# Kernel optimization log

Hardware: AMD Instinct MI355X
Metric: run time of the kernel (lower is better)

## Reference

```python
import jax, jax.numpy as jnp
import numpy as np

EPS = 1e-5


def _selective_scan(u, delta, A, Bm, Cm, D, delta_bias):
    # u, delta: (B, KD, L); A: (KD, N); Bm, Cm: (B, K, N, L); D, delta_bias: (KD,)
    Bb, KD, L = u.shape
    K = Bm.shape[1]
    Din = KD // K
    N = A.shape[1]
    delta = jax.nn.softplus(delta + delta_bias[None, :, None])            # (B,KD,L)
    dA = jnp.exp(delta[..., None] * A[None, :, None, :])                  # (B,KD,L,N)
    Bl = jnp.broadcast_to(Bm[:, :, None], (Bb, K, Din, N, L)).reshape(Bb, KD, N, L)
    Bl = jnp.moveaxis(Bl, -1, 2)                                          # (B,KD,L,N)
    dBu = (delta * u)[..., None] * Bl                                     # (B,KD,L,N)

    def comb(c1, c2):
        a1, b1 = c1
        a2, b2 = c2
        return a2 * a1, a2 * b1 + b2

    _, h = jax.lax.associative_scan(comb, (dA, dBu), axis=2)              # h: (B,KD,L,N)
    Cl = jnp.broadcast_to(Cm[:, :, None], (Bb, K, Din, N, L)).reshape(Bb, KD, N, L)
    Cl = jnp.moveaxis(Cl, -1, 2)
    y = jnp.sum(h * Cl, axis=-1) + D[None, :, None] * u                   # (B,KD,L)
    return y


def setup_inputs() -> dict:
    key = jax.random.key(0)
    ks = jax.random.split(key, 12)
    B, H, W, Dd = 1, 16, 16, 16
    C = 48            # d_model
    Din = 48          # d_inner (expand=1)
    N = 16            # d_state
    R = 3             # dt_rank = ceil(48/16)
    K = 8             # scan directions
    x = jax.random.normal(ks[0], (B, H, W, Dd, C), jnp.float32)
    in_proj_w = jax.random.normal(ks[1], (2 * Din, C), jnp.float32) * (C ** -0.5)
    conv_w = jax.random.normal(ks[2], (Din, 1, 3, 3, 3), jnp.float32) * 0.1
    conv_b = jax.random.normal(ks[3], (Din,), jnp.float32) * 0.01
    x_proj_weight = jax.random.normal(ks[4], (K, R + 2 * N, Din), jnp.float32) * (Din ** -0.5)
    dt_projs_weight = jax.random.uniform(ks[5], (K, Din, R), jnp.float32, -(R ** -0.5), R ** -0.5)
    # faithful dt bias init: inverse softplus of dt ~ logU(1e-3, 1e-1)
    u = jax.random.uniform(ks[6], (K, Din), jnp.float32)
    dt = jnp.exp(u * (np.log(0.1) - np.log(0.001)) + np.log(0.001))
    dt = jnp.clip(dt, 1e-4, None)
    dt_projs_bias = dt + jnp.log(-jnp.expm1(-dt))
    A_logs = jnp.log(jnp.broadcast_to(jnp.arange(1, N + 1, dtype=jnp.float32), (K * Din, N))).copy()
    Ds = jnp.ones((K * Din,), jnp.float32)
    norm_w = jnp.ones((Din,), jnp.float32)
    norm_b = jnp.zeros((Din,), jnp.float32)
    out_proj_w = jax.random.normal(ks[7], (C, Din), jnp.float32) * (Din ** -0.5)
    return {"x": x, "in_proj_w": in_proj_w, "conv_w": conv_w, "conv_b": conv_b,
            "x_proj_weight": x_proj_weight, "dt_projs_weight": dt_projs_weight,
            "dt_projs_bias": dt_projs_bias, "A_logs": A_logs, "Ds": Ds,
            "norm_w": norm_w, "norm_b": norm_b, "out_proj_w": out_proj_w}


def reference(x, in_proj_w, conv_w, conv_b, x_proj_weight, dt_projs_weight,
              dt_projs_bias, A_logs, Ds, norm_w, norm_b, out_proj_w):
    Bb, H, W, Dd, C = x.shape
    Din = in_proj_w.shape[0] // 2
    K = x_proj_weight.shape[0]
    R = dt_projs_weight.shape[2]
    N = A_logs.shape[1]
    L = H * W * Dd
    # in_proj and gate split
    xz = jnp.einsum('bhwdc,ec->bhwde', x, in_proj_w)
    xm, z = jnp.split(xz, 2, axis=-1)
    # depthwise 3D conv + SiLU (channels-first)
    xc = jnp.transpose(xm, (0, 4, 1, 2, 3))                               # (B,Din,H,W,D)
    xc = jax.lax.conv_general_dilated(xc, conv_w, (1, 1, 1), 'SAME',
                                      dimension_numbers=('NCDHW', 'OIDHW', 'NCDHW'),
                                      feature_group_count=Din)
    xc = jax.nn.silu(xc + conv_b[None, :, None, None, None])
    # 8 scan orderings: 4 axis permutations + their reversals
    x0 = xc.reshape(Bb, Din, L)
    x1 = jnp.transpose(xc, (0, 1, 3, 2, 4)).reshape(Bb, Din, L)
    x2 = jnp.transpose(xc, (0, 1, 4, 3, 2)).reshape(Bb, Din, L)
    x3 = jnp.transpose(xc, (0, 1, 2, 4, 3)).reshape(Bb, Din, L)
    x4s = jnp.stack([x0, x1, x2, x3], axis=1)                             # (B,4,Din,L)
    xs = jnp.concatenate([x4s, jnp.flip(x4s, axis=-1)], axis=1)           # (B,8,Din,L)
    # per-direction projections
    x_dbl = jnp.einsum('bkdl,kcd->bkcl', xs, x_proj_weight)
    dts, Bs, Cs = jnp.split(x_dbl, [R, R + N], axis=2)                    # (B,K,R,L),(B,K,N,L),(B,K,N,L)
    dts = jnp.einsum('bkrl,kdr->bkdl', dts, dt_projs_weight)              # (B,K,Din,L)
    u = xs.reshape(Bb, K * Din, L)
    delta = dts.reshape(Bb, K * Din, L)
    A = -jnp.exp(A_logs)                                                  # (K*Din, N)
    y = _selective_scan(u, delta, A, Bs, Cs, Ds, dt_projs_bias.reshape(-1))
    y = y.reshape(Bb, K, Din, L)
    # undo reversals and permutations, sum all directions
    yk = y[:, :4] + jnp.flip(y[:, 4:], axis=-1)                           # (B,4,Din,L)
    y0 = yk[:, 0].reshape(Bb, Din, H, W, Dd)
    y1 = jnp.transpose(yk[:, 1].reshape(Bb, Din, W, H, Dd), (0, 1, 3, 2, 4))
    y2 = jnp.transpose(yk[:, 2].reshape(Bb, Din, Dd, W, H), (0, 1, 4, 3, 2))
    y3 = jnp.transpose(yk[:, 3].reshape(Bb, Din, H, Dd, W), (0, 1, 2, 4, 3))
    ysum = y0 + y1 + y2 + y3                                              # (B,Din,H,W,D)
    # LayerNorm over channels, gate, out_proj
    yl = jnp.transpose(ysum, (0, 2, 3, 4, 1))                             # (B,H,W,D,Din)
    mu = jnp.mean(yl, axis=-1, keepdims=True)
    var = jnp.mean((yl - mu) ** 2, axis=-1, keepdims=True)
    yn = (yl - mu) * jax.lax.rsqrt(var + EPS) * norm_w + norm_b
    out = yn * jax.nn.silu(z)
    return jnp.einsum('bhwde,ce->bhwdc', out, out_proj_w)
```

## Files before the change

### kernel.cpp

```cpp
#include <hip/hip_runtime.h>
#include <hip/hip_bf16.h>
#include <math.h>

#define HH 16
#define WW 16
#define DD 16
#define LL 4096
#define CC 48
#define DIN 48
#define NN 16
#define RR 3
#define KK 8
#define KD 384
#define NCH 64
#define CHL 64

__device__ __forceinline__ float dpp_add(float x, const int ctrl_tag) {
    int xi = __float_as_int(x);
    int yi;
    switch (ctrl_tag) {
        case 0: yi = __builtin_amdgcn_update_dpp(0, xi, 0xB1, 0xF, 0xF, true); break;
        case 1: yi = __builtin_amdgcn_update_dpp(0, xi, 0x4E, 0xF, 0xF, true); break;
        case 2: yi = __builtin_amdgcn_update_dpp(0, xi, 0x124, 0xF, 0xF, true); break;
        default: yi = __builtin_amdgcn_update_dpp(0, xi, 0x128, 0xF, 0xF, true); break;
    }
    return x + __int_as_float(yi);
}
__device__ __forceinline__ float row16_sum(float p) {
    p = dpp_add(p, 0);
    p = dpp_add(p, 1);
    p = dpp_add(p, 2);
    p = dpp_add(p, 3);
    return p;
}

__global__ __launch_bounds__(256) void k_inproj(const float* __restrict__ x,
                                                const float* __restrict__ W,
                                                float* __restrict__ xm,
                                                float* __restrict__ z) {
    int tid = blockIdx.x * 256 + threadIdx.x;
    if (tid >= LL * 96) return;
    int e = tid % 96, l = tid / 96;
    const float4* xr = (const float4*)(x + l * CC);
    const float4* wr = (const float4*)(W + e * CC);
    float acc = 0.f;
#pragma unroll
    for (int c4 = 0; c4 < CC / 4; ++c4) {
        float4 a = xr[c4], b = wr[c4];
        acc += a.x * b.x + a.y * b.y + a.z * b.z + a.w * b.w;
    }
    if (e < DIN) xm[e * LL + l] = acc;
    else         z[l * DIN + (e - DIN)] = acc;
}

__global__ __launch_bounds__(256) void k_conv(const float* __restrict__ xm,
                                              const float* __restrict__ cw,
                                              const float* __restrict__ cb,
                                              float* __restrict__ xc) {
    int tid = blockIdx.x * 256 + threadIdx.x;
    if (tid >= DIN * LL) return;
    int s = tid & (LL - 1), d = tid >> 12;
    int dd = s & 15, w = (s >> 4) & 15, h = s >> 8;
    const float* wp = cw + d * 27;
    const float* xp = xm + d * LL;
    float acc = 0.f;
#pragma unroll
    for (int i = -1; i <= 1; ++i) {
        int hh = h + i; if (hh < 0 || hh > 15) continue;
#pragma unroll
        for (int j = -1; j <= 1; ++j) {
            int ww2 = w + j; if (ww2 < 0 || ww2 > 15) continue;
#pragma unroll
            for (int q = -1; q <= 1; ++q) {
                int dd2 = dd + q; if (dd2 < 0 || dd2 > 15) continue;
                acc += wp[(i + 1) * 9 + (j + 1) * 3 + (q + 1)]
                     * xp[hh * 256 + ww2 * 16 + dd2];
            }
        }
    }
    acc += cb[d];
    xc[tid] = acc / (1.f + __expf(-acc));
}

__global__ __launch_bounds__(768) void k_xscan1(const float* __restrict__ xc,
                                                const float* __restrict__ xpw,
                                                const float* __restrict__ dtw,
                                                const float* __restrict__ dtb,
                                                const float* __restrict__ A_logs,
                                                float* __restrict__ BC,
                                                float* __restrict__ ud_g,
                                                float* __restrict__ pa_g,
                                                float* __restrict__ hf_g) {
    int k = blockIdx.x >> 6;
    int c = blockIdx.x & (NCH - 1);
    int l0 = c * CHL;
    int tid = threadIdx.x;
    __shared__ float xt[48 * 68];
    __shared__ float xd[35 * 65];
    __shared__ float2 ud[48 * 68];
    int kperm = k & 3, krev = k & 4;
#pragma unroll
    for (int r = 0; r < 4; ++r) {
        int item = r * 768 + tid;
        int d = item >> 6, i = item & 63;
        int lg = l0 + i;
        int ll = krev ? (LL - 1 - lg) : lg;
        int a = ll >> 8, b2 = (ll >> 4) & 15, c2 = ll & 15;
        int src;
        switch (kperm) {
            case 0: src = ll;                       break;
            case 1: src = b2 * 256 + a * 16 + c2;   break;
            case 2: src = c2 * 256 + b2 * 16 + a;   break;
            default: src = a * 256 + c2 * 16 + b2;  break;
        }
        xt[d * 68 + i] = xc[d * LL + src];
    }
    __syncthreads();
    if (tid < 560) {
        int cc = tid % 35, l4 = tid / 35;
        const float* wr = xpw + (k * 35 + cc) * DIN;
        float4 acc = {0.f, 0.f, 0.f, 0.f};
#pragma unroll
        for (int d2 = 0; d2 < 48; ++d2) {
            float4 v = ((const float4*)(xt + d2 * 68))[l4];
            float w = wr[d2];
            acc.x += v.x * w; acc.y += v.y * w; acc.z += v.z * w; acc.w += v.w * w;
        }
        float* o = xd + cc * 65 + l4 * 4;
        o[0] = acc.x; o[1] = acc.y; o[2] = acc.z; o[3] = acc.w;
    }
    __syncthreads();
    if (tid < 512) {
        int l = tid >> 3, q = tid & 7;
        float4 v;
#pragma unroll
        for (int j = 0; j < 4; ++j) (&v.x)[j] = xd[(3 + q * 4 + j) * 65 + l];
        ((float4*)(BC + ((size_t)(k * LL + l0 + l)) * 32))[q] = v;
    }
#pragma unroll
    for (int r = 0; r < 4; ++r) {
        int item = r * 768 + tid;
        int d2 = item >> 6, l = item & 63;
        int gd = k * DIN + d2;
        float v = xd[l] * dtw[gd * 3] + xd[65 + l] * dtw[gd * 3 + 1]
                + xd[130 + l] * dtw[gd * 3 + 2] + dtb[gd];
        float sp = (v > 20.f) ? v : log1pf(__expf(v));
        float u = xt[d2 * 68 + l];
        float2 p = make_float2(u, sp);
        ud[d2 * 68 + l] = p;
        ((float2*)ud_g)[(size_t)gd * LL + l0 + l] = p;
    }
    __syncthreads();
    int d = tid >> 4, n = tid & 15;
    int gid = k * DIN + d;
    float A = -__expf(A_logs[gid * NN + n]);
    float h = 0.f, pa = 1.f;
#pragma unroll 8
    for (int i = 0; i < CHL; ++i) {
        float2 uv = ud[d * 68 + i];
        float Bv = xd[(3 + n) * 65 + i];
        float dA = __expf(uv.y * A);
        h = h * dA + uv.y * uv.x * Bv;
        pa *= dA;
    }
    size_t si = (size_t)gid * (NCH * 16) + c * 16 + n;
    pa_g[si] = pa;
    hf_g[si] = h;
}

__global__ __launch_bounds__(256) void k_scan2(const float* __restrict__ pa_g,
                                               const float* __restrict__ hf_g,
                                               float* __restrict__ h0_g) {
    int t = blockIdx.x * 256 + threadIdx.x;
    if (t >= KD * NN) return;
    int n = t & 15;
    int gid = t >> 4;
    size_t base = (size_t)gid * (NCH * 16) + n;
    float h = 0.f;
#pragma unroll 4
    for (int c = 0; c < NCH; ++c) {
        size_t idx = base + (size_t)c * 16;
        h0_g[idx] = h;
        h = h * pa_g[idx] + hf_g[idx];
    }
}

__global__ __launch_bounds__(768) void k_scan3(const float* __restrict__ ud_g,
                                               const float* __restrict__ BC,
                                               const float* __restrict__ A_logs,
                                               const float* __restrict__ Ds,
                                               const float* __restrict__ h0_g,
                                               float* __restrict__ y2) {
    int k = blockIdx.x >> 6;
    int c = blockIdx.x & (NCH - 1);
    int l0 = c * CHL;
    int tid = threadIdx.x;
    int d = tid >> 4, n = tid & 15;
    int gid = k * DIN + d;
    __shared__ float y_t[48 * 68];
    float A = -__expf(A_logs[gid * NN + n]);
    float Dv = Ds[gid];
    float h = h0_g[(size_t)gid * (NCH * 16) + c * 16 + n];
    const float2* up = ((const float2*)ud_g) + (size_t)gid * LL + l0;
    const float* bp = BC + ((size_t)(k * LL + l0)) * 32 + n;
    const float* cp = bp + 16;
#pragma unroll 8
    for (int i = 0; i < CHL; ++i) {
        float2 uv = up[i];
        float Bv = bp[(size_t)i * 32];
        float Cv = cp[(size_t)i * 32];
        float dA = __expf(uv.y * A);
        h = h * dA + uv.y * uv.x * Bv;
        float p = row16_sum(h * Cv);
        if (n == 0) y_t[d * 68 + i] = p + Dv * uv.x;
    }
    __syncthreads();
    {
        int g = tid >> 6, l = tid & 63;
        int lg = l0 + l;
        int ll = (k & 4) ? (LL - 1 - lg) : lg;
        int a = ll >> 8, b2 = (ll >> 4) & 15, c2 = ll & 15;
        int s;
        switch (k & 3) {
            case 0: s = ll;                        break;
            case 1: s = b2 * 256 + a * 16 + c2;    break;
            case 2: s = c2 * 256 + b2 * 16 + a;    break;
            default: s = a * 256 + c2 * 16 + b2;   break;
        }
        float4 v;
#pragma unroll
        for (int j = 0; j < 4; ++j) (&v.x)[j] = y_t[(g * 4 + j) * 68 + l];
        ((float4*)(y2 + (size_t)s * KD + k * DIN))[g] = v;
    }
}

__global__ __launch_bounds__(256) void k_final2(const float* __restrict__ y2,
                                                const float* __restrict__ z,
                                                const float* __restrict__ nw,
                                                const float* __restrict__ nb,
                                                const float* __restrict__ opw,
                                                float* __restrict__ out) {
    int wv = threadIdx.x >> 6, lane = threadIdx.x & 63;
    int s = blockIdx.x * 4 + wv;
    __shared__ float g[4][DIN];
    float val = 0.f;
    if (lane < DIN) {
        const float* yp = y2 + (size_t)s * KD + lane;
#pragma unroll
        for (int k = 0; k < KK; ++k) val += yp[k * DIN];
    }
    float m = val;
#pragma unroll
    for (int o = 32; o >= 1; o >>= 1) m += __shfl_xor(m, o, 64);
    m *= (1.f / 48.f);
    float dv = (lane < DIN) ? (val - m) : 0.f;
    float v2 = dv * dv;
#pragma unroll
    for (int o = 32; o >= 1; o >>= 1) v2 += __shfl_xor(v2, o, 64);
    v2 *= (1.f / 48.f);
    float inv = rsqrtf(v2 + 1e-5f);
    if (lane < DIN) {
        float yn = dv * inv * nw[lane] + nb[lane];
        float zz = z[s * DIN + lane];
        g[wv][lane] = yn * (zz / (1.f + __expf(-zz)));
    }
    __syncthreads();
    if (lane < DIN) {
        const float* wr = opw + lane * DIN;
        float acc = 0.f;
#pragma unroll
        for (int e = 0; e < DIN; ++e) acc += g[wv][e] * wr[e];
        out[s * CC + lane] = acc;
    }
}

extern "C" void kernel_launch(void* const* d_in, const int* in_sizes, int n_in,
                              void* d_out, int out_size, void* d_ws, size_t ws_size,
                              hipStream_t stream) {
    const float* x      = (const float*)d_in[0];
    const float* ipw    = (const float*)d_in[1];
    const float* cw     = (const float*)d_in[2];
    const float* cb     = (const float*)d_in[3];
    const float* xpw    = (const float*)d_in[4];
    const float* dtw    = (const float*)d_in[5];
    const float* dtb    = (const float*)d_in[6];
    const float* A_logs = (const float*)d_in[7];
    const float* Ds     = (const float*)d_in[8];
    const float* nw     = (const float*)d_in[9];
    const float* nb     = (const float*)d_in[10];
    const float* opw    = (const float*)d_in[11];
    float* out = (float*)d_out;

    float* ws   = (float*)d_ws;
    float* xm   = ws;
    float* z    = xm + DIN * LL;
    float* xc   = z + LL * DIN;
    float* ud_g = xc + DIN * LL;
    float* BC   = ud_g + (size_t)2 * KD * LL;
    float* y2   = BC + (size_t)KK * LL * 32;
    float* pa_g = y2 + (size_t)LL * KD;
    float* hf_g = pa_g + (size_t)KD * NCH * 16;
    float* h0_g = hf_g + (size_t)KD * NCH * 16;

    k_inproj<<<(LL * 96 + 255) / 256, 256, 0, stream>>>(x, ipw, xm, z);
    k_conv<<<(DIN * LL + 255) / 256, 256, 0, stream>>>(xm, cw, cb, xc);
    k_xscan1<<<KK * NCH, 768, 0, stream>>>(xc, xpw, dtw, dtb, A_logs,
                                           BC, ud_g, pa_g, hf_g);
    k_scan2<<<(KD * NN + 255) / 256, 256, 0, stream>>>(pa_g, hf_g, h0_g);
    k_scan3<<<KK * NCH, 768, 0, stream>>>(ud_g, BC, A_logs, Ds, h0_g, y2);
    k_final2<<<LL / 4, 256, 0, stream>>>(y2, z, nw, nb, opw, out);
}
```

Before: 155.0 us.

## Fuse all stages into one cooperative persistent kernel with grid syncs

Replaces six separate kernel launches with a single cooperative kernel of 512 blocks × 256 threads that runs in-projection, conv, x-projection plus chunk scan, the inter-chunk scan, the output scan and the final norm/gate/projection, separated by grid.sync. The scan's B/C and u/delta now stay in shared memory between the chunk-prefix pass and the output pass instead of going through global buffers, and each thread handles three channels rather than one. It is meant to remove launch overhead and global round-trips. In exchange it costs grid-wide barriers and less parallelism per stage, with a fallback to the old multi-kernel path if the cooperative launch fails.

```diff
diff --git a/kernel.cpp b/kernel.cpp
--- a/kernel.cpp
+++ b/kernel.cpp
@@ -1,6 +1,9 @@
 #include <hip/hip_runtime.h>
 #include <hip/hip_bf16.h>
+#include <hip/hip_cooperative_groups.h>
 #include <math.h>
+
+namespace cg = cooperative_groups;
 
 #define HH 16
 #define WW 16
@@ -14,6 +17,8 @@
 #define KD 384
 #define NCH 64
 #define CHL 64
+#define NBLK (KK * NCH)
+#define NTHR 256
 
 __device__ __forceinline__ float dpp_add(float x, const int ctrl_tag) {
     int xi = __float_as_int(x);
@@ -32,6 +37,279 @@
     p = dpp_add(p, 2);
     p = dpp_add(p, 3);
     return p;
+}
+
+__device__ __forceinline__ int perm_src(int kperm, int ll) {
+    int a = ll >> 8, b2 = (ll >> 4) & 15, c2 = ll & 15;
+    switch (kperm) {
+        case 0: return ll;
+        case 1: return b2 * 256 + a * 16 + c2;
+        case 2: return c2 * 256 + b2 * 16 + a;
+        default: return a * 256 + c2 * 16 + b2;
+    }
+}
+
+__global__ __launch_bounds__(NTHR) void k_all(const float* __restrict__ x,
+                                              const float* __restrict__ ipw,
+                                              const float* __restrict__ cw,
+                                              const float* __restrict__ cb,
+                                              const float* __restrict__ xpw,
+                                              const float* __restrict__ dtw,
+                                              const float* __restrict__ dtb,
+                                              const float* __restrict__ A_logs,
+                                              const float* __restrict__ Ds,
+                                              const float* __restrict__ nw,
+                                              const float* __restrict__ nb,
+                                              const float* __restrict__ opw,
+                                              float* __restrict__ out,
+                                              float* __restrict__ xm,
+                                              float* __restrict__ z,
+                                              float* __restrict__ xc,
+                                              float* __restrict__ y2,
+                                              float* __restrict__ pa_g,
+                                              float* __restrict__ hf_g,
+                                              float* __restrict__ h0_g) {
+    cg::grid_group grid = cg::this_grid();
+    int tid = threadIdx.x;
+    int bid = blockIdx.x;
+    __shared__ float xt[48 * 68];
+    __shared__ float xd[35 * 65];
+    __shared__ float2 ud[48 * 68];
+    __shared__ float gbuf[4][49];
+
+    {
+        int base = bid * 768;
+#pragma unroll
+        for (int r = 0; r < 3; ++r) {
+            int item = base + r * NTHR + tid;
+            int e = item % 96, l = item / 96;
+            const float4* xr = (const float4*)(x + l * CC);
+            const float4* wr = (const float4*)(ipw + e * CC);
+            float acc = 0.f;
+#pragma unroll
+            for (int c4 = 0; c4 < CC / 4; ++c4) {
+                float4 a = xr[c4], b = wr[c4];
+                acc += a.x * b.x + a.y * b.y + a.z * b.z + a.w * b.w;
+            }
+            if (e < DIN) xm[e * LL + l] = acc;
+            else         z[l * DIN + (e - DIN)] = acc;
+        }
+    }
+    grid.sync();
+
+    {
+        int base = bid * 384;
+#pragma unroll
+        for (int r = 0; r < 2; ++r) {
+            int li = r * NTHR + tid;
+            if (li < 384) {
+                int item = base + li;
+                int s = item & (LL - 1), d = item >> 12;
+                int dd = s & 15, w = (s >> 4) & 15, h = s >> 8;
+                const float* wp = cw + d * 27;
+                const float* xp = xm + d * LL;
+                float acc = 0.f;
+#pragma unroll
+                for (int i = -1; i <= 1; ++i) {
+                    int hh = h + i; if (hh < 0 || hh > 15) continue;
+#pragma unroll
+                    for (int j = -1; j <= 1; ++j) {
+                        int ww2 = w + j; if (ww2 < 0 || ww2 > 15) continue;
+#pragma unroll
+                        for (int q = -1; q <= 1; ++q) {
+                            int dd2 = dd + q; if (dd2 < 0 || dd2 > 15) continue;
+                            acc += wp[(i + 1) * 9 + (j + 1) * 3 + (q + 1)]
+                                 * xp[hh * 256 + ww2 * 16 + dd2];
+                        }
+                    }
+                }
+                acc += cb[d];
+                xc[item] = acc / (1.f + __expf(-acc));
+            }
+        }
+    }
+    grid.sync();
+
+    int k = bid >> 6;
+    int c = bid & (NCH - 1);
+    int l0 = c * CHL;
+    int kperm = k & 3, krev = k & 4;
+    {
+#pragma unroll
+        for (int r = 0; r < 12; ++r) {
+            int item = r * NTHR + tid;
+            int d = item >> 6, i = item & 63;
+            int lg = l0 + i;
+            int ll = krev ? (LL - 1 - lg) : lg;
+            xt[d * 68 + i] = xc[d * LL + perm_src(kperm, ll)];
+        }
+        __syncthreads();
+#pragma unroll
+        for (int r = 0; r < 3; ++r) {
+            int item = r * NTHR + tid;
+            if (item < 560) {
+                int cc = item % 35, l4 = item / 35;
+                const float* wr = xpw + (k * 35 + cc) * DIN;
+                float4 acc = {0.f, 0.f, 0.f, 0.f};
+#pragma unroll
+                for (int d2 = 0; d2 < 48; ++d2) {
+                    float4 v = ((const float4*)(xt + d2 * 68))[l4];
+                    float w = wr[d2];
+                    acc.x += v.x * w; acc.y += v.y * w; acc.z += v.z * w; acc.w += v.w * w;
+                }
+                float* o = xd + cc * 65 + l4 * 4;
+                o[0] = acc.x; o[1] = acc.y; o[2] = acc.z; o[3] = acc.w;
+            }
+        }
+        __syncthreads();
+#pragma unroll
+        for (int r = 0; r < 12; ++r) {
+            int item = r * NTHR + tid;
+            int d2 = item >> 6, l = item & 63;
+            int gd = k * DIN + d2;
+            float v = xd[l] * dtw[gd * 3] + xd[65 + l] * dtw[gd * 3 + 1]
+                    + xd[130 + l] * dtw[gd * 3 + 2] + dtb[gd];
+            float sp = (v > 20.f) ? v : log1pf(__expf(v));
+            ud[d2 * 68 + l] = make_float2(xt[d2 * 68 + l], sp);
+        }
+        __syncthreads();
+        int n = tid & 15, dbase = tid >> 4;
+        float A0 = -__expf(A_logs[(k * DIN + dbase) * NN + n]);
+        float A1 = -__expf(A_logs[(k * DIN + dbase + 16) * NN + n]);
+        float A2 = -__expf(A_logs[(k * DIN + dbase + 32) * NN + n]);
+        float h0v = 0.f, h1v = 0.f, h2v = 0.f;
+        float p0v = 1.f, p1v = 1.f, p2v = 1.f;
+#pragma unroll 4
+        for (int i = 0; i < CHL; ++i) {
+            float Bv = xd[(3 + n) * 65 + i];
+            float2 u0 = ud[dbase * 68 + i];
+            float2 u1 = ud[(dbase + 16) * 68 + i];
+            float2 u2 = ud[(dbase + 32) * 68 + i];
+            float dA0 = __expf(u0.y * A0);
+            float dA1 = __expf(u1.y * A1);
+            float dA2 = __expf(u2.y * A2);
+            h0v = h0v * dA0 + u0.y * u0.x * Bv;
+            h1v = h1v * dA1 + u1.y * u1.x * Bv;
+            h2v = h2v * dA2 + u2.y * u2.x * Bv;
+            p0v *= dA0; p1v *= dA1; p2v *= dA2;
+        }
+        pa_g[((size_t)(k * DIN + dbase) * 16 + n) * NCH + c] = p0v;
+        pa_g[((size_t)(k * DIN + dbase + 16) * 16 + n) * NCH + c] = p1v;
+        pa_g[((size_t)(k * DIN + dbase + 32) * 16 + n) * NCH + c] = p2v;
+        hf_g[((size_t)(k * DIN + dbase) * 16 + n) * NCH + c] = h0v;
+        hf_g[((size_t)(k * DIN + dbase + 16) * 16 + n) * NCH + c] = h1v;
+        hf_g[((size_t)(k * DIN + dbase + 32) * 16 + n) * NCH + c] = h2v;
+    }
+    grid.sync();
+
+    {
+        int wavebase = bid * 4 + (tid >> 6);
+        int lane = tid & 63;
+#pragma unroll
+        for (int j = 0; j < 3; ++j) {
+            int wid = j * 2048 + wavebase;
+            size_t idx = (size_t)wid * NCH + lane;
+            float a = pa_g[idx], b = hf_g[idx];
+#pragma unroll
+            for (int o = 1; o < 64; o <<= 1) {
+                float ap = __shfl_up(a, o, 64);
+                float bp = __shfl_up(b, o, 64);
+                if (lane >= o) { b = a * bp + b; a = a * ap; }
+            }
+            float h0 = __shfl_up(b, 1, 64);
+            if (lane == 0) h0 = 0.f;
+            h0_g[idx] = h0;
+        }
+    }
+    grid.sync();
+
+    {
+        int n = tid & 15, dbase = tid >> 4;
+        float A0 = -__expf(A_logs[(k * DIN + dbase) * NN + n]);
+        float A1 = -__expf(A_logs[(k * DIN + dbase + 16) * NN + n]);
+        float A2 = -__expf(A_logs[(k * DIN + dbase + 32) * NN + n]);
+        float D0 = Ds[k * DIN + dbase];
+        float D1 = Ds[k * DIN + dbase + 16];
+        float D2 = Ds[k * DIN + dbase + 32];
+        float h0v = h0_g[((size_t)(k * DIN + dbase) * 16 + n) * NCH + c];
+        float h1v = h0_g[((size_t)(k * DIN + dbase + 16) * 16 + n) * NCH + c];
+        float h2v = h0_g[((size_t)(k * DIN + dbase + 32) * 16 + n) * NCH + c];
+        float* y_t = xt;
+#pragma unroll 4
+        for (int i = 0; i < CHL; ++i) {
+            float Bv = xd[(3 + n) * 65 + i];
+            float Cv = xd[(19 + n) * 65 + i];
+            float2 u0 = ud[dbase * 68 + i];
+            float2 u1 = ud[(dbase + 16) * 68 + i];
+            float2 u2 = ud[(dbase + 32) * 68 + i];
+            float dA0 = __expf(u0.y * A0);
+            float dA1 = __expf(u1.y * A1);
+            float dA2 = __expf(u2.y * A2);
+            h0v = h0v * dA0 + u0.y * u0.x * Bv;
+            h1v = h1v * dA1 + u1.y * u1.x * Bv;
+            h2v = h2v * dA2 + u2.y * u2.x * Bv;
+            float s0 = row16_sum(h0v * Cv);
+            float s1 = row16_sum(h1v * Cv);
+            float s2 = row16_sum(h2v * Cv);
+            if (n == 0) {
+                y_t[dbase * 68 + i] = s0 + D0 * u0.x;
+                y_t[(dbase + 16) * 68 + i] = s1 + D1 * u1.x;
+                y_t[(dbase + 32) * 68 + i] = s2 + D2 * u2.x;
+            }
+        }
+        __syncthreads();
+#pragma unroll
+        for (int r = 0; r < 3; ++r) {
+            int item = r * NTHR + tid;
+            int g = item >> 6, l = item & 63;
+            int lg = l0 + l;
+            int ll = krev ? (LL - 1 - lg) : lg;
+            int s = perm_src(kperm, ll);
+            float4 v;
+#pragma unroll
+            for (int j = 0; j < 4; ++j) (&v.x)[j] = y_t[(g * 4 + j) * 68 + l];
+            ((float4*)(y2 + (size_t)s * KD + k * DIN))[g] = v;
+        }
+    }
+    grid.sync();
+
+    {
+        int wv = tid >> 6, lane = tid & 63;
+#pragma unroll
+        for (int r = 0; r < 2; ++r) {
+            int s = bid * 8 + wv * 2 + r;
+            float val = 0.f;
+            if (lane < DIN) {
+                const float* yp = y2 + (size_t)s * KD + lane;
+#pragma unroll
+                for (int kk = 0; kk < KK; ++kk) val += yp[kk * DIN];
+            }
+            float m = val;
+#pragma unroll
+            for (int o = 32; o >= 1; o >>= 1) m += __shfl_xor(m, o, 64);
+            m *= (1.f / 48.f);
+            float dv = (lane < DIN) ? (val - m) : 0.f;
+            float v2 = dv * dv;
+#pragma unroll
+            for (int o = 32; o >= 1; o >>= 1) v2 += __shfl_xor(v2, o, 64);
+            v2 *= (1.f / 48.f);
+            float inv = rsqrtf(v2 + 1e-5f);
+            if (lane < DIN) {
+                float yn = dv * inv * nw[lane] + nb[lane];
+                float zz = z[s * DIN + lane];
+                gbuf[wv][lane] = yn * (zz / (1.f + __expf(-zz)));
+            }
+            __syncthreads();
+            if (lane < DIN) {
+                const float* wr = opw + lane * DIN;
+                float acc = 0.f;
+#pragma unroll
+                for (int e = 0; e < DIN; ++e) acc += gbuf[wv][e] * wr[e];
+                out[s * CC + lane] = acc;
+            }
+            __syncthreads();
+        }
+    }
 }
 
 __global__ __launch_bounds__(256) void k_inproj(const float* __restrict__ x,
@@ -105,15 +383,7 @@
         int d = item >> 6, i = item & 63;
         int lg = l0 + i;
         int ll = krev ? (LL - 1 - lg) : lg;
-        int a = ll >> 8, b2 = (ll >> 4) & 15, c2 = ll & 15;
-        int src;
-        switch (kperm) {
-            case 0: src = ll;                       break;
-            case 1: src = b2 * 256 + a * 16 + c2;   break;
-            case 2: src = c2 * 256 + b2 * 16 + a;   break;
-            default: src = a * 256 + c2 * 16 + b2;  break;
-        }
-        xt[d * 68 + i] = xc[d * LL + src];
+        xt[d * 68 + i] = xc[d * LL + perm_src(kperm, ll)];
     }
     __syncthreads();
     if (tid < 560) {
@@ -215,23 +485,14 @@
         if (n == 0) y_t[d * 68 + i] = p + Dv * uv.x;
     }
     __syncthreads();
-    {
-        int g = tid >> 6, l = tid & 63;
-        int lg = l0 + l;
-        int ll = (k & 4) ? (LL - 1 - lg) : lg;
-        int a = ll >> 8, b2 = (ll >> 4) & 15, c2 = ll & 15;
-        int s;
-        switch (k & 3) {
-            case 0: s = ll;                        break;
-            case 1: s = b2 * 256 + a * 16 + c2;    break;
-            case 2: s = c2 * 256 + b2 * 16 + a;    break;
-            default: s = a * 256 + c2 * 16 + b2;   break;
-        }
-        float4 v;
-#pragma unroll
-        for (int j = 0; j < 4; ++j) (&v.x)[j] = y_t[(g * 4 + j) * 68 + l];
-        ((float4*)(y2 + (size_t)s * KD + k * DIN))[g] = v;
-    }
+    int g = tid >> 6, l = tid & 63;
+    int lg = l0 + l;
+    int ll = (k & 4) ? (LL - 1 - lg) : lg;
+    int s = perm_src(k & 3, ll);
+    float4 v;
+#pragma unroll
+    for (int j = 0; j < 4; ++j) (&v.x)[j] = y_t[(g * 4 + j) * 68 + l];
+    ((float4*)(y2 + (size_t)s * KD + k * DIN))[g] = v;
 }
 
 __global__ __launch_bounds__(256) void k_final2(const float* __restrict__ y2,
@@ -295,18 +556,28 @@
     float* xm   = ws;
     float* z    = xm + DIN * LL;
     float* xc   = z + LL * DIN;
-    float* ud_g = xc + DIN * LL;
-    float* BC   = ud_g + (size_t)2 * KD * LL;
-    float* y2   = BC + (size_t)KK * LL * 32;
+    float* y2   = xc + DIN * LL;
     float* pa_g = y2 + (size_t)LL * KD;
     float* hf_g = pa_g + (size_t)KD * NCH * 16;
     float* h0_g = hf_g + (size_t)KD * NCH * 16;
-
-    k_inproj<<<(LL * 96 + 255) / 256, 256, 0, stream>>>(x, ipw, xm, z);
-    k_conv<<<(DIN * LL + 255) / 256, 256, 0, stream>>>(xm, cw, cb, xc);
-    k_xscan1<<<KK * NCH, 768, 0, stream>>>(xc, xpw, dtw, dtb, A_logs,
-                                           BC, ud_g, pa_g, hf_g);
-    k_scan2<<<(KD * NN + 255) / 256, 256, 0, stream>>>(pa_g, hf_g, h0_g);
-    k_scan3<<<KK * NCH, 768, 0, stream>>>(ud_g, BC, A_logs, Ds, h0_g, y2);
-    k_final2<<<LL / 4, 256, 0, stream>>>(y2, z, nw, nb, opw, out);
-}
+    float* ud_g = h0_g + (size_t)KD * NCH * 16;
+    float* BC   = ud_g + (size_t)2 * KD * LL;
+
+    void* args[] = {
+        (void*)&x, (void*)&ipw, (void*)&cw, (void*)&cb, (void*)&xpw,
+        (void*)&dtw, (void*)&dtb, (void*)&A_logs, (void*)&Ds, (void*)&nw,
+        (void*)&nb, (void*)&opw, (void*)&out, (void*)&xm, (void*)&z,
+        (void*)&xc, (void*)&y2, (void*)&pa_g, (void*)&hf_g, (void*)&h0_g
+    };
+    hipError_t err = hipLaunchCooperativeKernel((void*)k_all, dim3(NBLK),
+                                                dim3(NTHR), args, 0, stream);
+    if (err != hipSuccess) {
+        k_inproj<<<(LL * 96 + 255) / 256, 256, 0, stream>>>(x, ipw, xm, z);
+        k_conv<<<(DIN * LL + 255) / 256, 256, 0, stream>>>(xm, cw, cb, xc);
+        k_xscan1<<<KK * NCH, 768, 0, stream>>>(xc, xpw, dtw, dtb, A_logs,
+                                               BC, ud_g, pa_g, hf_g);
+        k_scan2<<<(KD * NN + 255) / 256, 256, 0, stream>>>(pa_g, hf_g, h0_g);
+        k_scan3<<<KK * NCH, 768, 0, stream>>>(ud_g, BC, A_logs, Ds, h0_g, y2);
+        k_final2<<<LL / 4, 256, 0, stream>>>(y2, z, nw, nb, opw, out);
+    }
+}
```

After: 464.1 us. +199.4%, slower.

## Recompute x_proj tiles in scan phase and fold carry propagation into it

Applied to the files above, without the earlier changes.

Both scan kernels now rebuild the gathered input tile, the x_proj output and the softplus delta in shared memory instead of the first kernel writing B/C, u and delta to global memory for the second to read back. The separate inter-chunk carry kernel is removed. Each block of the second scan now serially combines the per-chunk (pa, hf) summaries of all earlier chunks to get its initial state. This removes one launch and a large global round trip. In exchange the projection work is done twice and later chunks do up to 63 serial carry steps, which makes the work uneven across blocks.

```diff
diff --git a/kernel.cpp b/kernel.cpp
--- a/kernel.cpp
+++ b/kernel.cpp
@@ -34,6 +34,58 @@
     return p;
 }
 
+__device__ __forceinline__ int perm_src(int kperm, int ll) {
+    int a = ll >> 8, b2 = (ll >> 4) & 15, c2 = ll & 15;
+    switch (kperm) {
+        case 0: return ll;
+        case 1: return b2 * 256 + a * 16 + c2;
+        case 2: return c2 * 256 + b2 * 16 + a;
+        default: return a * 256 + c2 * 16 + b2;
+    }
+}
+
+__device__ __forceinline__ void build_tiles(const float* __restrict__ xc,
+                                            const float* __restrict__ xpw,
+                                            const float* __restrict__ dtw,
+                                            const float* __restrict__ dtb,
+                                            int k, int l0, int kperm, int krev,
+                                            int tid,
+                                            float* xt, float* xd, float* dt) {
+#pragma unroll
+    for (int r = 0; r < 4; ++r) {
+        int item = r * 768 + tid;
+        int d = item >> 6, i = item & 63;
+        int lg = l0 + i;
+        int ll = krev ? (LL - 1 - lg) : lg;
+        xt[d * 68 + i] = xc[d * LL + perm_src(kperm, ll)];
+    }
+    __syncthreads();
+    if (tid < 560) {
+        int cc = tid % 35, l4 = tid / 35;
+        const float* wr = xpw + (k * 35 + cc) * DIN;
+        float4 acc = {0.f, 0.f, 0.f, 0.f};
+#pragma unroll
+        for (int d2 = 0; d2 < 48; ++d2) {
+            float4 v = ((const float4*)(xt + d2 * 68))[l4];
+            float w = wr[d2];
+            acc.x += v.x * w; acc.y += v.y * w; acc.z += v.z * w; acc.w += v.w * w;
+        }
+        float* o = xd + cc * 65 + l4 * 4;
+        o[0] = acc.x; o[1] = acc.y; o[2] = acc.z; o[3] = acc.w;
+    }
+    __syncthreads();
+#pragma unroll
+    for (int r = 0; r < 4; ++r) {
+        int item = r * 768 + tid;
+        int d2 = item >> 6, l = item & 63;
+        int gd = k * DIN + d2;
+        float v = xd[l] * dtw[gd * 3] + xd[65 + l] * dtw[gd * 3 + 1]
+                + xd[130 + l] * dtw[gd * 3 + 2] + dtb[gd];
+        dt[d2 * 68 + l] = (v > 20.f) ? v : log1pf(__expf(v));
+    }
+    __syncthreads();
+}
+
 __global__ __launch_bounds__(256) void k_inproj(const float* __restrict__ x,
                                                 const float* __restrict__ W,
                                                 float* __restrict__ xm,
@@ -82,151 +134,84 @@
     xc[tid] = acc / (1.f + __expf(-acc));
 }
 
-__global__ __launch_bounds__(768) void k_xscan1(const float* __restrict__ xc,
-                                                const float* __restrict__ xpw,
-                                                const float* __restrict__ dtw,
-                                                const float* __restrict__ dtb,
-                                                const float* __restrict__ A_logs,
-                                                float* __restrict__ BC,
-                                                float* __restrict__ ud_g,
-                                                float* __restrict__ pa_g,
-                                                float* __restrict__ hf_g) {
+__global__ __launch_bounds__(768) void k_scanA(const float* __restrict__ xc,
+                                               const float* __restrict__ xpw,
+                                               const float* __restrict__ dtw,
+                                               const float* __restrict__ dtb,
+                                               const float* __restrict__ A_logs,
+                                               float* __restrict__ pa_g,
+                                               float* __restrict__ hf_g) {
     int k = blockIdx.x >> 6;
     int c = blockIdx.x & (NCH - 1);
     int l0 = c * CHL;
     int tid = threadIdx.x;
     __shared__ float xt[48 * 68];
     __shared__ float xd[35 * 65];
-    __shared__ float2 ud[48 * 68];
-    int kperm = k & 3, krev = k & 4;
-#pragma unroll
-    for (int r = 0; r < 4; ++r) {
-        int item = r * 768 + tid;
-        int d = item >> 6, i = item & 63;
-        int lg = l0 + i;
-        int ll = krev ? (LL - 1 - lg) : lg;
-        int a = ll >> 8, b2 = (ll >> 4) & 15, c2 = ll & 15;
-        int src;
-        switch (kperm) {
-            case 0: src = ll;                       break;
-            case 1: src = b2 * 256 + a * 16 + c2;   break;
-            case 2: src = c2 * 256 + b2 * 16 + a;   break;
-            default: src = a * 256 + c2 * 16 + b2;  break;
-        }
-        xt[d * 68 + i] = xc[d * LL + src];
-    }
-    __syncthreads();
-    if (tid < 560) {
-        int cc = tid % 35, l4 = tid / 35;
-        const float* wr = xpw + (k * 35 + cc) * DIN;
-        float4 acc = {0.f, 0.f, 0.f, 0.f};
-#pragma unroll
-        for (int d2 = 0; d2 < 48; ++d2) {
-            float4 v = ((const float4*)(xt + d2 * 68))[l4];
-            float w = wr[d2];
-            acc.x += v.x * w; acc.y += v.y * w; acc.z += v.z * w; acc.w += v.w * w;
-        }
-        float* o = xd + cc * 65 + l4 * 4;
-        o[0] = acc.x; o[1] = acc.y; o[2] = acc.z; o[3] = acc.w;
-    }
-    __syncthreads();
-    if (tid < 512) {
-        int l = tid >> 3, q = tid & 7;
-        float4 v;
-#pragma unroll
-        for (int j = 0; j < 4; ++j) (&v.x)[j] = xd[(3 + q * 4 + j) * 65 + l];
-        ((float4*)(BC + ((size_t)(k * LL + l0 + l)) * 32))[q] = v;
-    }
-#pragma unroll
-    for (int r = 0; r < 4; ++r) {
-        int item = r * 768 + tid;
-        int d2 = item >> 6, l = item & 63;
-        int gd = k * DIN + d2;
-        float v = xd[l] * dtw[gd * 3] + xd[65 + l] * dtw[gd * 3 + 1]
-                + xd[130 + l] * dtw[gd * 3 + 2] + dtb[gd];
-        float sp = (v > 20.f) ? v : log1pf(__expf(v));
-        float u = xt[d2 * 68 + l];
-        float2 p = make_float2(u, sp);
-        ud[d2 * 68 + l] = p;
-        ((float2*)ud_g)[(size_t)gd * LL + l0 + l] = p;
-    }
-    __syncthreads();
+    __shared__ float dt[48 * 68];
+    build_tiles(xc, xpw, dtw, dtb, k, l0, k & 3, k & 4, tid, xt, xd, dt);
     int d = tid >> 4, n = tid & 15;
     int gid = k * DIN + d;
     float A = -__expf(A_logs[gid * NN + n]);
     float h = 0.f, pa = 1.f;
 #pragma unroll 8
     for (int i = 0; i < CHL; ++i) {
-        float2 uv = ud[d * 68 + i];
+        float delta = dt[d * 68 + i];
+        float u = xt[d * 68 + i];
         float Bv = xd[(3 + n) * 65 + i];
-        float dA = __expf(uv.y * A);
-        h = h * dA + uv.y * uv.x * Bv;
+        float dA = __expf(delta * A);
+        h = h * dA + delta * u * Bv;
         pa *= dA;
     }
-    size_t si = (size_t)gid * (NCH * 16) + c * 16 + n;
+    size_t si = ((size_t)c * KK + k) * 768 + tid;
     pa_g[si] = pa;
     hf_g[si] = h;
 }
 
-__global__ __launch_bounds__(256) void k_scan2(const float* __restrict__ pa_g,
-                                               const float* __restrict__ hf_g,
-                                               float* __restrict__ h0_g) {
-    int t = blockIdx.x * 256 + threadIdx.x;
-    if (t >= KD * NN) return;
-    int n = t & 15;
-    int gid = t >> 4;
-    size_t base = (size_t)gid * (NCH * 16) + n;
-    float h = 0.f;
-#pragma unroll 4
-    for (int c = 0; c < NCH; ++c) {
-        size_t idx = base + (size_t)c * 16;
-        h0_g[idx] = h;
-        h = h * pa_g[idx] + hf_g[idx];
-    }
-}
-
-__global__ __launch_bounds__(768) void k_scan3(const float* __restrict__ ud_g,
-                                               const float* __restrict__ BC,
+__global__ __launch_bounds__(768) void k_scanB(const float* __restrict__ xc,
+                                               const float* __restrict__ xpw,
+                                               const float* __restrict__ dtw,
+                                               const float* __restrict__ dtb,
                                                const float* __restrict__ A_logs,
                                                const float* __restrict__ Ds,
-                                               const float* __restrict__ h0_g,
+                                               const float* __restrict__ pa_g,
+                                               const float* __restrict__ hf_g,
                                                float* __restrict__ y2) {
     int k = blockIdx.x >> 6;
     int c = blockIdx.x & (NCH - 1);
     int l0 = c * CHL;
     int tid = threadIdx.x;
+    int kperm = k & 3, krev = k & 4;
+    __shared__ float xt[48 * 68];
+    __shared__ float xd[35 * 65];
+    __shared__ float dt[48 * 68];
+    __shared__ float y_t[48 * 68];
+    build_tiles(xc, xpw, dtw, dtb, k, l0, kperm, krev, tid, xt, xd, dt);
+    float h = 0.f;
+    for (int cc = 0; cc < c; ++cc) {
+        size_t idx = ((size_t)cc * KK + k) * 768 + tid;
+        h = pa_g[idx] * h + hf_g[idx];
+    }
     int d = tid >> 4, n = tid & 15;
     int gid = k * DIN + d;
-    __shared__ float y_t[48 * 68];
     float A = -__expf(A_logs[gid * NN + n]);
     float Dv = Ds[gid];
-    float h = h0_g[(size_t)gid * (NCH * 16) + c * 16 + n];
-    const float2* up = ((const float2*)ud_g) + (size_t)gid * LL + l0;
-    const float* bp = BC + ((size_t)(k * LL + l0)) * 32 + n;
-    const float* cp = bp + 16;
 #pragma unroll 8
     for (int i = 0; i < CHL; ++i) {
-        float2 uv = up[i];
-        float Bv = bp[(size_t)i * 32];
-        float Cv = cp[(size_t)i * 32];
-        float dA = __expf(uv.y * A);
-        h = h * dA + uv.y * uv.x * Bv;
+        float delta = dt[d * 68 + i];
+        float u = xt[d * 68 + i];
+        float Bv = xd[(3 + n) * 65 + i];
+        float Cv = xd[(19 + n) * 65 + i];
+        float dA = __expf(delta * A);
+        h = h * dA + delta * u * Bv;
         float p = row16_sum(h * Cv);
-        if (n == 0) y_t[d * 68 + i] = p + Dv * uv.x;
+        if (n == 0) y_t[d * 68 + i] = p + Dv * u;
     }
     __syncthreads();
     {
         int g = tid >> 6, l = tid & 63;
         int lg = l0 + l;
-        int ll = (k & 4) ? (LL - 1 - lg) : lg;
-        int a = ll >> 8, b2 = (ll >> 4) & 15, c2 = ll & 15;
-        int s;
-        switch (k & 3) {
-            case 0: s = ll;                        break;
-            case 1: s = b2 * 256 + a * 16 + c2;    break;
-            case 2: s = c2 * 256 + b2 * 16 + a;    break;
-            default: s = a * 256 + c2 * 16 + b2;   break;
-        }
+        int ll = krev ? (LL - 1 - lg) : lg;
+        int s = perm_src(kperm, ll);
         float4 v;
 #pragma unroll
         for (int j = 0; j < 4; ++j) (&v.x)[j] = y_t[(g * 4 + j) * 68 + l];
@@ -295,18 +280,14 @@
     float* xm   = ws;
     float* z    = xm + DIN * LL;
     float* xc   = z + LL * DIN;
-    float* ud_g = xc + DIN * LL;
-    float* BC   = ud_g + (size_t)2 * KD * LL;
-    float* y2   = BC + (size_t)KK * LL * 32;
+    float* y2   = xc + DIN * LL;
     float* pa_g = y2 + (size_t)LL * KD;
-    float* hf_g = pa_g + (size_t)KD * NCH * 16;
-    float* h0_g = hf_g + (size_t)KD * NCH * 16;
+    float* hf_g = pa_g + (size_t)NCH * KK * 768;
 
     k_inproj<<<(LL * 96 + 255) / 256, 256, 0, stream>>>(x, ipw, xm, z);
     k_conv<<<(DIN * LL + 255) / 256, 256, 0, stream>>>(xm, cw, cb, xc);
-    k_xscan1<<<KK * NCH, 768, 0, stream>>>(xc, xpw, dtw, dtb, A_logs,
-                                           BC, ud_g, pa_g, hf_g);
-    k_scan2<<<(KD * NN + 255) / 256, 256, 0, stream>>>(pa_g, hf_g, h0_g);
-    k_scan3<<<KK * NCH, 768, 0, stream>>>(ud_g, BC, A_logs, Ds, h0_g, y2);
+    k_scanA<<<KK * NCH, 768, 0, stream>>>(xc, xpw, dtw, dtb, A_logs, pa_g, hf_g);
+    k_scanB<<<KK * NCH, 768, 0, stream>>>(xc, xpw, dtw, dtb, A_logs, Ds,
+                                          pa_g, hf_g, y2);
     k_final2<<<LL / 4, 256, 0, stream>>>(y2, z, nw, nb, opw, out);
 }
```

New measurement: 180.5 us. 1.16x slower.
